# Kernel optimization log

Measured on AMD Instinct MI355X. Metric: run time of the kernel, lower is better.

## Reference

```python
import jax, jax.numpy as jnp
import numpy as np

D_MODEL = 1024
N_HEADS = 16
D_FF = 4 * D_MODEL
CTX = 2048
EPS = 1e-5


def setup_inputs() -> dict:
    key = jax.random.key(0)
    ks = jax.random.split(key, 8)
    s = 0.02
    z = jax.random.normal(ks[0], (2, CTX, D_MODEL), dtype=jnp.float32)
    W_Q = jax.random.normal(ks[1], (D_MODEL, D_MODEL), dtype=jnp.float32) * s
    W_K = jax.random.normal(ks[2], (D_MODEL, D_MODEL), dtype=jnp.float32) * s
    W_V = jax.random.normal(ks[3], (D_MODEL, D_MODEL), dtype=jnp.float32) * s
    W_O = jax.random.normal(ks[4], (D_MODEL, D_MODEL), dtype=jnp.float32) * s
    W_fc = jax.random.normal(ks[5], (D_MODEL, D_FF), dtype=jnp.float32) * s
    W_proj = jax.random.normal(ks[6], (D_FF, D_MODEL), dtype=jnp.float32) * s
    g1 = jnp.ones((D_MODEL,), dtype=jnp.float32)
    g2 = jnp.ones((D_MODEL,), dtype=jnp.float32)
    return {"z": z, "W_Q": W_Q, "W_K": W_K, "W_V": W_V, "W_O": W_O,
            "W_fc": W_fc, "W_proj": W_proj, "g1": g1, "g2": g2}


def rmsnorm(x, gain):
    rms = jnp.sqrt(jnp.sum(x * x, axis=-1, keepdims=True) / x.shape[-1] + EPS)
    return (x / rms) * gain


def gelu_erf(x):
    return x * 0.5 * (1.0 + jax.lax.erf(x / jnp.sqrt(2.0).astype(x.dtype)))


def attention(zn, W_Q, W_K, W_V, W_O):
    B, T, D = zn.shape
    H = N_HEADS
    dh = D // H
    # [B,T,D] -> [B,H,T,dh]
    def split(x):
        return x.reshape(B, T, H, dh).transpose(0, 2, 1, 3)
    Q = split(zn @ W_Q)
    K = split(zn @ W_K)
    V = split(zn @ W_V)
    scores = jnp.einsum('bhtd,bhsd->bhts', Q, K) / jnp.sqrt(jnp.float32(dh))
    causal = jnp.triu(jnp.ones((T, T), dtype=bool), k=1)  # True above diagonal -> masked
    scores = jnp.where(causal[None, None], -jnp.inf, scores)
    weights = jax.nn.softmax(scores, axis=-1)
    ctx = jnp.einsum('bhts,bhsd->bhtd', weights, V)
    ctx = ctx.transpose(0, 2, 1, 3).reshape(B, T, D)
    return ctx @ W_O


def reference(z, W_Q, W_K, W_V, W_O, W_fc, W_proj, g1, g2):
    # pre-norm GPT block: z + attn(norm1(z)); then + ffn(norm2(z))
    z = z + attention(rmsnorm(z, g1), W_Q, W_K, W_V, W_O)
    h = rmsnorm(z, g2)
    ffn = gelu_erf(h @ W_fc) @ W_proj
    return z + ffn
```

## Files before the change

### kernel.cpp

```cpp
#include <hip/hip_runtime.h>
#include <hip/hip_bf16.h>
#include <math.h>


typedef __bf16 bf16x8 __attribute__((ext_vector_type(8)));
typedef float  f32x4  __attribute__((ext_vector_type(4)));

#define MFMA_16x16x32_BF16(A, B, C) __builtin_amdgcn_mfma_f32_16x16x32_bf16((A), (B), (C), 0, 0, 0)

#define GLDS16(g, l) __builtin_amdgcn_global_load_lds( \
    (const __attribute__((address_space(1))) void*)(g), \
    (__attribute__((address_space(3))) void*)(l), 16, 0, 0)

__global__ __launch_bounds__(256) void fused_head_kernel(
    const float* __restrict__ W_Q, const float* __restrict__ W_K,
    const float* __restrict__ W_V, const float* __restrict__ W_O,
    const float* __restrict__ W_fc, const float* __restrict__ W_proj,
    __bf16* __restrict__ WtQKV, __bf16* __restrict__ WtO,
    __bf16* __restrict__ Wtfc, __bf16* __restrict__ Wtproj,
    const float* __restrict__ z, const float* __restrict__ g1,
    __bf16* __restrict__ zn)
{
    const int id = blockIdx.x;
    if (id >= 12288) {
        const int row = id - 12288, t = threadIdx.x;
        const float4 v = ((const float4*)(z + (size_t)row * 1024))[t];
        float ss = v.x * v.x + v.y * v.y + v.z * v.z + v.w * v.w;
#pragma unroll
        for (int m = 1; m < 64; m <<= 1) ss += __shfl_xor(ss, m);
        __shared__ float red[4];
        const int wid = t >> 6, lane = t & 63;
        if (lane == 0) red[wid] = ss;
        __syncthreads();
        const float tot = red[0] + red[1] + red[2] + red[3];
        const float inv = rsqrtf(tot * (1.0f / 1024.0f) + 1e-5f);
        const float4 gv = ((const float4*)g1)[t];
        __bf16* o = zn + (size_t)row * 1024 + t * 4;
        o[0] = (__bf16)(v.x * inv * gv.x);
        o[1] = (__bf16)(v.y * inv * gv.y);
        o[2] = (__bf16)(v.z * inv * gv.z);
        o[3] = (__bf16)(v.w * inv * gv.w);
        return;
    }
    const float* src;
    __bf16* dst;
    int K, N, nx, t;
    if (id < 4096) {
        const int wsel = id >> 10;
        t = id & 1023;
        src = (wsel == 0) ? W_Q : (wsel == 1) ? W_K : (wsel == 2) ? W_V : W_O;
        dst = (wsel < 3) ? (WtQKV + (size_t)wsel * 1048576) : WtO;
        K = 1024; N = 1024; nx = 32;
    } else if (id < 8192) {
        t = id - 4096; src = W_fc; dst = Wtfc; K = 1024; N = 4096; nx = 128;
    } else {
        t = id - 8192; src = W_proj; dst = Wtproj; K = 4096; N = 1024; nx = 32;
    }
    const int n0 = (t % nx) * 32, k0 = (t / nx) * 32;

    __shared__ float tile[32][33];
    const int c = threadIdx.x & 31, r = threadIdx.x >> 5;
#pragma unroll
    for (int i = 0; i < 4; ++i)
        tile[r + 8 * i][c] = src[(size_t)(k0 + r + 8 * i) * N + n0 + c];
    __syncthreads();
#pragma unroll
    for (int i = 0; i < 4; ++i)
        dst[(size_t)(n0 + r + 8 * i) * K + k0 + c] = (__bf16)tile[c][r + 8 * i];
}

__global__ __launch_bounds__(256) void rmsnorm_kernel(
    const float* __restrict__ x, const float* __restrict__ gain,
    __bf16* __restrict__ out)
{
    const int row = blockIdx.x, t = threadIdx.x;
    const float4 v = ((const float4*)(x + (size_t)row * 1024))[t];
    float ss = v.x * v.x + v.y * v.y + v.z * v.z + v.w * v.w;
#pragma unroll
    for (int m = 1; m < 64; m <<= 1) ss += __shfl_xor(ss, m);
    __shared__ float red[4];
    const int wid = t >> 6, lane = t & 63;
    if (lane == 0) red[wid] = ss;
    __syncthreads();
    const float tot = red[0] + red[1] + red[2] + red[3];
    const float inv = rsqrtf(tot * (1.0f / 1024.0f) + 1e-5f);
    const float4 gv = ((const float4*)gain)[t];
    __bf16* o = out + (size_t)row * 1024 + t * 4;
    o[0] = (__bf16)(v.x * inv * gv.x);
    o[1] = (__bf16)(v.y * inv * gv.y);
    o[2] = (__bf16)(v.z * inv * gv.z);
    o[3] = (__bf16)(v.w * inv * gv.w);
}

__global__ __launch_bounds__(256) void reduce_add_kernel(
    float* __restrict__ out, const float* __restrict__ p0,
    const float* __restrict__ p1, int n4)
{
    for (int i = blockIdx.x * 256 + threadIdx.x; i < n4; i += gridDim.x * 256) {
        const float4 a = ((const float4*)p0)[i];
        const float4 b = ((const float4*)p1)[i];
        float4 o = ((float4*)out)[i];
        o.x += a.x + b.x; o.y += a.y + b.y;
        o.z += a.z + b.z; o.w += a.w + b.w;
        ((float4*)out)[i] = o;
    }
}

template <int EPI>
__device__ __forceinline__ void epi_write(
    void* outp, const float* res, int N, int rowg, int colg, float v)
{
    if constexpr (EPI == 1) {
        const size_t idx = (size_t)rowg * N + colg;
        ((float*)outp)[idx] = res[idx] + v;
    } else if constexpr (EPI == 2) {
        const size_t idx = (size_t)rowg * N + colg;
        const float u = v * (1.0f + 0.044715f * v * v) * 2.3022585093f;
        const float r = __builtin_amdgcn_rcpf(1.0f + exp2f(u));
        ((__bf16*)outp)[idx] = (__bf16)(v - v * r);
    } else if constexpr (EPI == 3) {
        const size_t idx = (size_t)rowg * N + colg;
        ((float*)outp)[idx] += v;
    } else {
        __bf16* base = (__bf16*)outp;
        const int seg = colg >> 10;
        const int cg = colg & 1023;
        if (seg < 2) {
            base[(size_t)seg * 4194304 + (size_t)rowg * 1024 + cg] = (__bf16)v;
        } else {
            const int tt = rowg & 2047;
            const int r32 = tt & 31;
            const int p = ((r32 & 12) << 1) | ((r32 >> 2) & 4) | (r32 & 3);
            base[8388608 +
                 ((size_t)((rowg >> 11) * 16 + (cg >> 6)) * 64 + (cg & 63)) * 2048 +
                 ((tt & ~31) | p)] = (__bf16)v;
        }
    }
}

template <int EPI>
__global__ __launch_bounds__(512, 2) void gemm256(
    const __bf16* __restrict__ A, const __bf16* __restrict__ Bt,
    void* __restrict__ outp, const float* __restrict__ res,
    int M, int N, int K)
{
    __shared__ __bf16 As[2][2][128 * 64];
    __shared__ __bf16 Bs[2][2][128 * 64];
    const int tid = threadIdx.x;

    const int gx = gridDim.x, nwg = gx * gridDim.y;
    int bid = blockIdx.y * gx + blockIdx.x;
    if ((nwg & 7) == 0) bid = (bid & 7) * (nwg >> 3) + (bid >> 3);
    const int m0 = (bid / gx) * 256, n0 = (bid % gx) * 256;

    const int lane = tid & 63, w = tid >> 6;
    const int wr = w >> 2, wc = w & 3;
    const int lr = lane & 15, g = lane >> 4;
    const int srow8 = lane >> 3, schunk = (lane & 7) ^ srow8;
    const int xk = lr & 7;
    const int wch = wc >> 1, bro = (wc & 1) * 64;

    const __bf16* Ab = A + (size_t)m0 * K;
    const __bf16* Bb = Bt + (size_t)n0 * K;

    auto STG = [&](const __bf16* gb, __bf16* lds, int kt, int half) {
        const __bf16* src = gb + (size_t)(half * 128) * K + (kt << 6);
#pragma unroll
        for (int j = 0; j < 2; ++j) {
            const int sidx = j * 8 + w;
            GLDS16(src + (size_t)(sidx * 8 + srow8) * K + schunk * 8, lds + sidx * 512);
        }
    };

    f32x4 acc[8][4] = {};
    bf16x8 af[2][4], bf[2][4];

#define LAF(BUF, QM) do {                                                       \
    _Pragma("unroll") for (int i_ = 0; i_ < 4; ++i_)                            \
    _Pragma("unroll") for (int kk_ = 0; kk_ < 2; ++kk_)                         \
        af[kk_][i_] = *(const bf16x8*)&As[BUF][wr]                              \
            [((QM) * 64 + i_ * 16 + lr) * 64 + (((kk_ * 4 + g) ^ xk) << 3)];    \
    } while (0)

#define LBF(BUF, QN) do {                                                       \
    _Pragma("unroll") for (int i_ = 0; i_ < 2; ++i_)                            \
    _Pragma("unroll") for (int kk_ = 0; kk_ < 2; ++kk_)                         \
        bf[kk_][(QN) * 2 + i_] = *(const bf16x8*)&Bs[BUF][wch]                  \
            [(bro + ((QN) * 2 + i_) * 16 + lr) * 64 + (((kk_ * 4 + g) ^ xk) << 3)]; \
    } while (0)

#define MMQ(QM, QN) do {                                                        \
    __builtin_amdgcn_s_setprio(1);                                              \
    _Pragma("unroll") for (int kk_ = 0; kk_ < 2; ++kk_)                         \
    _Pragma("unroll") for (int i_ = 0; i_ < 4; ++i_)                            \
    _Pragma("unroll") for (int n_ = 0; n_ < 2; ++n_)                            \
        acc[(QM) * 4 + i_][(QN) * 2 + n_] = MFMA_16x16x32_BF16(                 \
            af[kk_][i_], bf[kk_][(QN) * 2 + n_], acc[(QM) * 4 + i_][(QN) * 2 + n_]); \
    __builtin_amdgcn_s_setprio(0);                                              \
    } while (0)

#define BAR()  __builtin_amdgcn_s_barrier()
#define VMC(N_) asm volatile("s_waitcnt vmcnt(" #N_ ")" ::: "memory")
#define SGB0() __builtin_amdgcn_sched_barrier(0)

    const int nt = K >> 6, niter = nt >> 1;

    STG(Ab, &As[0][0][0], 0, 0); STG(Ab, &As[0][1][0], 0, 1);
    STG(Bb, &Bs[0][0][0], 0, 0); STG(Bb, &Bs[0][1][0], 0, 1);
    STG(Bb, &Bs[1][0][0], 1, 0); STG(Bb, &Bs[1][1][0], 1, 1);

    for (int i = 0; i < niter - 1; ++i) {
        const int t1 = 2 * i + 1;
        STG(Ab, &As[1][0][0], t1, 0);
        VMC(6); BAR(); SGB0();
        LAF(0, 0); LBF(0, 0); MMQ(0, 0); BAR();
        LBF(0, 1); STG(Ab, &As[1][1][0], t1, 1); BAR(); MMQ(0, 1); BAR();
        LAF(0, 1); STG(Bb, &Bs[0][0][0], t1 + 1, 0); BAR(); MMQ(1, 0); BAR();
        STG(Bb, &Bs[0][1][0], t1 + 1, 1); BAR(); MMQ(1, 1); BAR();
        STG(Ab, &As[0][0][0], t1 + 1, 0);
        VMC(6); BAR(); SGB0();
        LAF(1, 0); LBF(1, 0); MMQ(0, 0); BAR();
        LBF(1, 1); STG(Ab, &As[0][1][0], t1 + 1, 1); BAR(); MMQ(0, 1); BAR();
        LAF(1, 1); STG(Bb, &Bs[1][0][0], t1 + 2, 0); BAR(); MMQ(1, 0); BAR();
        STG(Bb, &Bs[1][1][0], t1 + 2, 1); BAR(); MMQ(1, 1); BAR();
    }
    {
        STG(Ab, &As[1][0][0], nt - 1, 0);
        VMC(6); BAR(); SGB0();
        LAF(0, 0); LBF(0, 0); MMQ(0, 0); BAR();
        LBF(0, 1); STG(Ab, &As[1][1][0], nt - 1, 1); BAR(); MMQ(0, 1); BAR();
        LAF(0, 1); BAR(); MMQ(1, 0); BAR();
        BAR(); MMQ(1, 1); BAR();
        VMC(0); BAR(); SGB0();
        LAF(1, 0); LBF(1, 0); MMQ(0, 0); BAR();
        LBF(1, 1); BAR(); MMQ(0, 1); BAR();
        LAF(1, 1); BAR(); MMQ(1, 0); BAR();
        BAR(); MMQ(1, 1); BAR();
    }
#undef LAF
#undef LBF
#undef MMQ
#undef BAR
#undef VMC
#undef SGB0

#pragma unroll
    for (int mi = 0; mi < 8; ++mi)
#pragma unroll
        for (int ni = 0; ni < 4; ++ni) {
            const int colg = n0 + wc * 64 + ni * 16 + lr;
#pragma unroll
            for (int r = 0; r < 4; ++r) {
                const int rowg = m0 + wr * 128 + mi * 16 + 4 * g + r;
                epi_write<EPI>(outp, res, N, rowg, colg, acc[mi][ni][r]);
            }
        }
}

template <int BM, int BN, int EPI>
__global__ __launch_bounds__(256) void gemm_bf16(
    const __bf16* __restrict__ A, const __bf16* __restrict__ Bt,
    void* __restrict__ outp, const float* __restrict__ res,
    int M, int N, int K, int Kld)
{
    __shared__ __bf16 As[2][BM * 64];
    __shared__ __bf16 Bs[2][BN * 64];
    const int tid = threadIdx.x;

    const int gx = gridDim.x, nwg = gx * gridDim.y;
    int bid = blockIdx.y * gx + blockIdx.x;
    if ((nwg & 7) == 0) bid = (bid & 7) * (nwg >> 3) + (bid >> 3);
    const int m0 = (bid / gx) * BM, n0 = (bid % gx) * BN;

    const int lane = tid & 63, w = tid >> 6;
    const int wm = w >> 1, wn = w & 1;
    const int lr = lane & 15, g = lane >> 4;
    const int srow = lane >> 3;
    const int scol = ((lane & 7) ^ srow) * 8;
    const int xr8 = lr & 7;

    constexpr int MI = BM / 32, NI = BN / 32;
    f32x4 acc[MI][NI] = {};

    const __bf16* Abase = A + (size_t)m0 * Kld + blockIdx.z * K;
    const __bf16* Bbase = Bt + (size_t)n0 * Kld + blockIdx.z * K;

    auto STAGE = [&](int kb, int buf) {
#pragma unroll
        for (int j = 0; j < BM / 32; ++j) {
            const int s = j * 4 + w;
            GLDS16(Abase + (size_t)(s * 8 + srow) * Kld + kb + scol, &As[buf][s * 512]);
        }
#pragma unroll
        for (int j = 0; j < BN / 32; ++j) {
            const int s = j * 4 + w;
            GLDS16(Bbase + (size_t)(s * 8 + srow) * Kld + kb + scol, &Bs[buf][s * 512]);
        }
    };

    const int nt = K >> 6;
    STAGE(0, 0);
    __syncthreads();

    for (int t = 0; t < nt; ++t) {
        const int cur = t & 1;
        if (t + 1 < nt) STAGE((t + 1) << 6, cur ^ 1);

        bf16x8 af[2][MI], bfr[2][NI];
#pragma unroll
        for (int kk = 0; kk < 2; ++kk) {
#pragma unroll
            for (int i = 0; i < MI; ++i)
                af[kk][i] = *(const bf16x8*)
                    &As[cur][(wm * (BM / 2) + i * 16 + lr) * 64 + (((kk * 4 + g) ^ xr8) << 3)];
#pragma unroll
            for (int i = 0; i < NI; ++i)
                bfr[kk][i] = *(const bf16x8*)
                    &Bs[cur][(wn * (BN / 2) + i * 16 + lr) * 64 + (((kk * 4 + g) ^ xr8) << 3)];
        }
#pragma unroll
        for (int kk = 0; kk < 2; ++kk)
#pragma unroll
            for (int mi = 0; mi < MI; ++mi)
#pragma unroll
                for (int ni = 0; ni < NI; ++ni)
                    acc[mi][ni] = MFMA_16x16x32_BF16(af[kk][mi], bfr[kk][ni], acc[mi][ni]);
        if (t + 1 < nt) __syncthreads();
    }

#pragma unroll
    for (int mi = 0; mi < MI; ++mi)
#pragma unroll
        for (int ni = 0; ni < NI; ++ni) {
            const int colg = n0 + wn * (BN / 2) + ni * 16 + lr;
#pragma unroll
            for (int r = 0; r < 4; ++r) {
                const int rowg = m0 + wm * (BM / 2) + mi * 16 + 4 * g + r;
                const float v = acc[mi][ni][r];
                if constexpr (EPI == 5) {
                    float* pout = (blockIdx.z == 0) ? (float*)outp : (float*)(void*)res;
                    pout[(size_t)rowg * N + colg] = v;
                } else {
                    epi_write<EPI>(outp, res, N, rowg, colg, v);
                }
            }
        }
}

__global__ __launch_bounds__(512) void attn_kernel(
    const __bf16* __restrict__ Q, const __bf16* __restrict__ Kb,
    const __bf16* __restrict__ Vt, __bf16* __restrict__ ctx)
{
    const int Dm = 1024, T = 2048;
    const int tid = threadIdx.x;
    const int w = tid >> 6, lane = tid & 63;
    const int lr = lane & 15, g = lane >> 4;
    const int bx = blockIdx.x;
    const int j = bx >> 5, bh = bx & 31, b = bh >> 4, h = bh & 15;
    const int qc = (j < 8) ? j : 23 - j;
    const int qbase = qc * 128 + w * 16;
    const size_t rowoff = (size_t)b * T;
    const __bf16* Qp = Q + rowoff * Dm + h * 64;
    const __bf16* Kp = Kb + rowoff * Dm + h * 64;
    const __bf16* Vtp = Vt + (size_t)bh * 64 * 2048;

    __shared__ __bf16 Ks[2][128 * 64];
    __shared__ __bf16 Vs[2][64 * 128];

    bf16x8 qf0 = *(const bf16x8*)&Qp[(size_t)(qbase + lr) * Dm + g * 8];
    bf16x8 qf1 = *(const bf16x8*)&Qp[(size_t)(qbase + lr) * Dm + 32 + g * 8];
    const float qsc = 0.125f * 1.44269504088896340736f;
#pragma unroll
    for (int jj = 0; jj < 8; ++jj) {
        qf0[jj] = (__bf16)((float)qf0[jj] * qsc);
        qf1[jj] = (__bf16)((float)qf1[jj] * qsc);
    }

    const int ksrow = lane >> 3;
    const int kschunk = (lane & 7) ^ ksrow;
    const int vsrow = lane >> 4;

    f32x4 acc[4] = {};
    float m_s = -__builtin_inff(), l_s = 0.0f;
    const int nsteps = qc + 1;
    const f32x4 zacc = {0.0f, 0.0f, 0.0f, 0.0f};
    const int x8 = lr & 7;
    const int qg = qbase + lr;

    auto STAGE = [&](int kvb, int buf) {
#pragma unroll
        for (int jj = 0; jj < 2; ++jj) {
            const int krow = w * 16 + jj * 8;
            GLDS16(Kp + (size_t)(kvb + krow + ksrow) * Dm + kschunk * 8,
                   &Ks[buf][krow * 64]);
            const int vrow = w * 8 + jj * 4;
            const int vchunk = (lane & 15) ^ ((vrow + vsrow) & 15);
            GLDS16(Vtp + (size_t)(vrow + vsrow) * T + kvb + vchunk * 8,
                   &Vs[buf][vrow * 128]);
        }
    };

    STAGE(0, 0);
    __syncthreads();

    for (int t = 0; t < nsteps; ++t) {
        const int kvb = t * 128, cur = t & 1;
        if (t + 1 < nsteps) STAGE(kvb + 128, cur ^ 1);

        float sv[8][4];
#pragma unroll
        for (int s4 = 0; s4 < 8; ++s4) {
            const int kv0 = kvb + s4 * 16;
            if (kv0 <= qbase + 15) {
                const int row = s4 * 16 + lr;
                const bf16x8 kfa = *(const bf16x8*)&Ks[cur][row * 64 + ((g ^ x8) << 3)];
                const bf16x8 kfb = *(const bf16x8*)&Ks[cur][row * 64 + (((4 + g) ^ x8) << 3)];
                f32x4 st = MFMA_16x16x32_BF16(kfa, qf0, zacc);
                st = MFMA_16x16x32_BF16(kfb, qf1, st);
                const bool domask = (kv0 + 15 > qbase);
#pragma unroll
                for (int r = 0; r < 4; ++r) {
                    float x = st[r];
                    if (domask && (kv0 + 4 * g + r > qg)) x = -__builtin_inff();
                    sv[s4][r] = x;
                }
            } else {
#pragma unroll
                for (int r = 0; r < 4; ++r) sv[s4][r] = -__builtin_inff();
            }
        }

        float tm = sv[0][0];
#pragma unroll
        for (int s4 = 0; s4 < 8; ++s4)
#pragma unroll
            for (int r = 0; r < 4; ++r) tm = fmaxf(tm, sv[s4][r]);
        tm = fmaxf(tm, __shfl_xor(tm, 16));
        tm = fmaxf(tm, __shfl_xor(tm, 32));

        float m_use = m_s;
        if (!__all(tm - m_s <= 11.5f)) {
            m_use = fmaxf(m_s, tm);
            const float corr = exp2f(m_s - m_use);
            l_s *= corr;
            float cr[4];
#pragma unroll
            for (int r = 0; r < 4; ++r) cr[r] = __shfl(corr, 4 * g + r);
#pragma unroll
            for (int ct = 0; ct < 4; ++ct) {
                acc[ct][0] *= cr[0]; acc[ct][1] *= cr[1];
                acc[ct][2] *= cr[2]; acc[ct][3] *= cr[3];
            }
            m_s = m_use;
        }

        float rs = 0.0f;
#pragma unroll
        for (int s4 = 0; s4 < 8; ++s4)
#pragma unroll
            for (int r = 0; r < 4; ++r) {
                sv[s4][r] = exp2f(sv[s4][r] - m_use);
                rs += sv[s4][r];
            }
        rs += __shfl_xor(rs, 16);
        rs += __shfl_xor(rs, 32);
        l_s += rs;

        bf16x8 pa[4];
#pragma unroll
        for (int s = 0; s < 4; ++s)
#pragma unroll
            for (int r = 0; r < 4; ++r) {
                pa[s][r] = (__bf16)sv[2 * s][r];
                pa[s][4 + r] = (__bf16)sv[2 * s + 1][r];
            }
#pragma unroll
        for (int ct = 0; ct < 4; ++ct) {
            const __bf16* vrow = &Vs[cur][(ct * 16 + lr) * 128];
#pragma unroll
            for (int s = 0; s < 4; ++s) {
                if (kvb + s * 32 <= qbase + 15) {
                    const bf16x8 vf =
                        *(const bf16x8*)&vrow[(((s * 4 + g) ^ lr) << 3)];
                    acc[ct] = MFMA_16x16x32_BF16(pa[s], vf, acc[ct]);
                }
            }
        }
        __syncthreads();
    }

    const float il = __builtin_amdgcn_rcpf(l_s);
    float dn[4];
#pragma unroll
    for (int r = 0; r < 4; ++r) dn[r] = __shfl(il, 4 * g + r);
#pragma unroll
    for (int ct = 0; ct < 4; ++ct)
#pragma unroll
        for (int r = 0; r < 4; ++r)
            ctx[(rowoff + qbase + 4 * g + r) * Dm + h * 64 + ct * 16 + lr] =
                (__bf16)(acc[ct][r] * dn[r]);
}

extern "C" void kernel_launch(void* const* d_in, const int* in_sizes, int n_in,
                              void* d_out, int out_size, void* d_ws, size_t ws_size,
                              hipStream_t stream)
{
    (void)in_sizes; (void)n_in; (void)out_size; (void)ws_size;
    const float* z      = (const float*)d_in[0];
    const float* W_Q    = (const float*)d_in[1];
    const float* W_K    = (const float*)d_in[2];
    const float* W_V    = (const float*)d_in[3];
    const float* W_O    = (const float*)d_in[4];
    const float* W_fc   = (const float*)d_in[5];
    const float* W_proj = (const float*)d_in[6];
    const float* g1     = (const float*)d_in[7];
    const float* g2     = (const float*)d_in[8];
    float* out = (float*)d_out;

    char* ws = (char*)d_ws;
    const size_t MB = (size_t)1 << 20;
    __bf16* WtQKV  = (__bf16*)(ws + 0 * MB);
    __bf16* WtO    = (__bf16*)(ws + 6 * MB);
    __bf16* Wtfc   = (__bf16*)(ws + 8 * MB);
    __bf16* Wtproj = (__bf16*)(ws + 16 * MB);
    __bf16* zn     = (__bf16*)(ws + 24 * MB);
    __bf16* Qb     = (__bf16*)(ws + 32 * MB);
    __bf16* Kbuf   = (__bf16*)(ws + 40 * MB);
    __bf16* Vtb    = (__bf16*)(ws + 48 * MB);
    __bf16* ffn1   = (__bf16*)(ws + 40 * MB);
    float*  part0  = (float*)(ws + 0 * MB);
    float*  part1  = (float*)(ws + 24 * MB);
    __bf16* ctx    = zn;
    __bf16* hb     = Qb;

    const int Tt = 2048, Dm = 1024, Bb = 2, M = Bb * Tt, DFF = 4096;
    const dim3 blk256(256), blk512(512);

    fused_head_kernel<<<16384, blk256, 0, stream>>>(
        W_Q, W_K, W_V, W_O, W_fc, W_proj, WtQKV, WtO, Wtfc, Wtproj, z, g1, zn);

    gemm_bf16<128, 128, 4><<<dim3(24, 32), blk256, 0, stream>>>(
        zn, WtQKV, Qb, nullptr, M, 3072, Dm, Dm);

    attn_kernel<<<512, blk512, 0, stream>>>(Qb, Kbuf, Vtb, ctx);

    gemm_bf16<128, 64, 1><<<dim3(16, 32), blk256, 0, stream>>>(
        ctx, WtO, out, z, M, Dm, Dm, Dm);

    rmsnorm_kernel<<<M, blk256, 0, stream>>>(out, g2, hb);

    gemm256<2><<<dim3(16, 16), blk512, 0, stream>>>(
        hb, Wtfc, ffn1, nullptr, M, DFF, Dm);

    gemm_bf16<128, 128, 5><<<dim3(8, 32, 2), blk256, 0, stream>>>(
        ffn1, Wtproj, part0, (const float*)part1, M, Dm, DFF / 2, DFF);

    reduce_add_kernel<<<2048, blk256, 0, stream>>>(out, part0, part1, M * Dm / 4);
}
```

Measured before the change: 246.4 us.

## Replace split-K partial buffers with atomic adds and specialize unmasked attention tiles

```diff
diff --git a/kernel.cpp b/kernel.cpp
--- a/kernel.cpp
+++ b/kernel.cpp
@@ -92,20 +92,6 @@
     o[3] = (__bf16)(v.w * inv * gv.w);
 }
 
-__global__ __launch_bounds__(256) void reduce_add_kernel(
-    float* __restrict__ out, const float* __restrict__ p0,
-    const float* __restrict__ p1, int n4)
-{
-    for (int i = blockIdx.x * 256 + threadIdx.x; i < n4; i += gridDim.x * 256) {
-        const float4 a = ((const float4*)p0)[i];
-        const float4 b = ((const float4*)p1)[i];
-        float4 o = ((float4*)out)[i];
-        o.x += a.x + b.x; o.y += a.y + b.y;
-        o.z += a.z + b.z; o.w += a.w + b.w;
-        ((float4*)out)[i] = o;
-    }
-}
-
 template <int EPI>
 __device__ __forceinline__ void epi_write(
     void* outp, const float* res, int N, int rowg, int colg, float v)
@@ -118,9 +104,8 @@
         const float u = v * (1.0f + 0.044715f * v * v) * 2.3022585093f;
         const float r = __builtin_amdgcn_rcpf(1.0f + exp2f(u));
         ((__bf16*)outp)[idx] = (__bf16)(v - v * r);
-    } else if constexpr (EPI == 3) {
-        const size_t idx = (size_t)rowg * N + colg;
-        ((float*)outp)[idx] += v;
+    } else if constexpr (EPI == 6) {
+        unsafeAtomicAdd(&((float*)outp)[(size_t)rowg * N + colg], v);
     } else {
         __bf16* base = (__bf16*)outp;
         const int seg = colg >> 10;
@@ -336,13 +321,7 @@
 #pragma unroll
             for (int r = 0; r < 4; ++r) {
                 const int rowg = m0 + wm * (BM / 2) + mi * 16 + 4 * g + r;
-                const float v = acc[mi][ni][r];
-                if constexpr (EPI == 5) {
-                    float* pout = (blockIdx.z == 0) ? (float*)outp : (float*)(void*)res;
-                    pout[(size_t)rowg * N + colg] = v;
-                } else {
-                    epi_write<EPI>(outp, res, N, rowg, colg, v);
-                }
+                epi_write<EPI>(outp, res, N, rowg, colg, acc[mi][ni][r]);
             }
         }
 }
@@ -408,25 +387,38 @@
         if (t + 1 < nsteps) STAGE(kvb + 128, cur ^ 1);
 
         float sv[8][4];
-#pragma unroll
-        for (int s4 = 0; s4 < 8; ++s4) {
-            const int kv0 = kvb + s4 * 16;
-            if (kv0 <= qbase + 15) {
+        if (t < qc) {
+#pragma unroll
+            for (int s4 = 0; s4 < 8; ++s4) {
                 const int row = s4 * 16 + lr;
                 const bf16x8 kfa = *(const bf16x8*)&Ks[cur][row * 64 + ((g ^ x8) << 3)];
                 const bf16x8 kfb = *(const bf16x8*)&Ks[cur][row * 64 + (((4 + g) ^ x8) << 3)];
                 f32x4 st = MFMA_16x16x32_BF16(kfa, qf0, zacc);
                 st = MFMA_16x16x32_BF16(kfb, qf1, st);
-                const bool domask = (kv0 + 15 > qbase);
-#pragma unroll
-                for (int r = 0; r < 4; ++r) {
-                    float x = st[r];
-                    if (domask && (kv0 + 4 * g + r > qg)) x = -__builtin_inff();
-                    sv[s4][r] = x;
+#pragma unroll
+                for (int r = 0; r < 4; ++r) sv[s4][r] = st[r];
+            }
+        } else {
+#pragma unroll
+            for (int s4 = 0; s4 < 8; ++s4) {
+                const int kv0 = kvb + s4 * 16;
+                if (kv0 <= qbase + 15) {
+                    const int row = s4 * 16 + lr;
+                    const bf16x8 kfa = *(const bf16x8*)&Ks[cur][row * 64 + ((g ^ x8) << 3)];
+                    const bf16x8 kfb = *(const bf16x8*)&Ks[cur][row * 64 + (((4 + g) ^ x8) << 3)];
+                    f32x4 st = MFMA_16x16x32_BF16(kfa, qf0, zacc);
+                    st = MFMA_16x16x32_BF16(kfb, qf1, st);
+                    const bool domask = (kv0 + 15 > qbase);
+#pragma unroll
+                    for (int r = 0; r < 4; ++r) {
+                        float x = st[r];
+                        if (domask && (kv0 + 4 * g + r > qg)) x = -__builtin_inff();
+                        sv[s4][r] = x;
+                    }
+                } else {
+#pragma unroll
+                    for (int r = 0; r < 4; ++r) sv[s4][r] = -__builtin_inff();
                 }
-            } else {
-#pragma unroll
-                for (int r = 0; r < 4; ++r) sv[s4][r] = -__builtin_inff();
             }
         }
 
@@ -474,15 +466,26 @@
                 pa[s][r] = (__bf16)sv[2 * s][r];
                 pa[s][4 + r] = (__bf16)sv[2 * s + 1][r];
             }
-#pragma unroll
-        for (int ct = 0; ct < 4; ++ct) {
-            const __bf16* vrow = &Vs[cur][(ct * 16 + lr) * 128];
-#pragma unroll
-            for (int s = 0; s < 4; ++s) {
-                if (kvb + s * 32 <= qbase + 15) {
-                    const bf16x8 vf =
-                        *(const bf16x8*)&vrow[(((s * 4 + g) ^ lr) << 3)];
+        if (t < qc) {
+#pragma unroll
+            for (int ct = 0; ct < 4; ++ct) {
+                const __bf16* vrow = &Vs[cur][(ct * 16 + lr) * 128];
+#pragma unroll
+                for (int s = 0; s < 4; ++s) {
+                    const bf16x8 vf = *(const bf16x8*)&vrow[(((s * 4 + g) ^ lr) << 3)];
                     acc[ct] = MFMA_16x16x32_BF16(pa[s], vf, acc[ct]);
+                }
+            }
+        } else {
+#pragma unroll
+            for (int ct = 0; ct < 4; ++ct) {
+                const __bf16* vrow = &Vs[cur][(ct * 16 + lr) * 128];
+#pragma unroll
+                for (int s = 0; s < 4; ++s) {
+                    if (kvb + s * 32 <= qbase + 15) {
+                        const bf16x8 vf = *(const bf16x8*)&vrow[(((s * 4 + g) ^ lr) << 3)];
+                        acc[ct] = MFMA_16x16x32_BF16(pa[s], vf, acc[ct]);
+                    }
                 }
             }
         }
@@ -528,8 +531,6 @@
     __bf16* Kbuf   = (__bf16*)(ws + 40 * MB);
     __bf16* Vtb    = (__bf16*)(ws + 48 * MB);
     __bf16* ffn1   = (__bf16*)(ws + 40 * MB);
-    float*  part0  = (float*)(ws + 0 * MB);
-    float*  part1  = (float*)(ws + 24 * MB);
     __bf16* ctx    = zn;
     __bf16* hb     = Qb;
 
@@ -552,8 +553,6 @@
     gemm256<2><<<dim3(16, 16), blk512, 0, stream>>>(
         hb, Wtfc, ffn1, nullptr, M, DFF, Dm);
 
-    gemm_bf16<128, 128, 5><<<dim3(8, 32, 2), blk256, 0, stream>>>(
-        ffn1, Wtproj, part0, (const float*)part1, M, Dm, DFF / 2, DFF);
-
-    reduce_add_kernel<<<2048, blk256, 0, stream>>>(out, part0, part1, M * Dm / 4);
-}
+    gemm_bf16<128, 128, 6><<<dim3(8, 32, 2), blk256, 0, stream>>>(
+        ffn1, Wtproj, out, nullptr, M, Dm, DFF / 2, DFF);
+}
```

Result: no change. 246.1 us (-0.1%).
